# Kernel tuning notes

Measured on AMD Instinct MI355X. Metric: run time of the kernel, lower is better.

The kernel has to match this reference:

```python
import jax, jax.numpy as jnp
import numpy as np

N_NODES = 100_000
N_EDGES = 1_600_000
F_IN = 128
NHID = 128
G = 64            # num graphs in the batch
N_CLASSES = 2
EMB = NHID * 6    # embedding_data dim so concat dim == NHID*8


def _lin_init(k, fi, fo):
    s = 1.0 / np.sqrt(fi)
    k1, k2 = jax.random.split(k)
    w = jax.random.uniform(k1, (fi, fo), jnp.float32, -s, s)
    b = jax.random.uniform(k2, (fo,), jnp.float32, -s, s)
    return w, b


def setup_inputs() -> dict:
    key = jax.random.key(0)
    ks = jax.random.split(key, 12)
    x = jax.random.normal(ks[0], (N_NODES, F_IN), jnp.float32)
    edge_index = jax.random.randint(ks[1], (2, N_EDGES), 0, N_NODES, dtype=jnp.int32)
    per = N_NODES // G
    batch = jnp.minimum(jnp.arange(N_NODES, dtype=jnp.int32) // per, G - 1)  # sorted, even split
    embedding_data = jax.random.normal(ks[2], (G, EMB), jnp.float32)
    conv_w, conv_b = _lin_init(ks[3], F_IN, NHID)
    lin0_w, lin0_b = _lin_init(ks[4], F_IN, NHID)
    lin1_w, lin1_b = _lin_init(ks[5], NHID * 8, NHID * 4)
    lin2_w, lin2_b = _lin_init(ks[6], NHID * 4, NHID * 2)
    lin3_w, lin3_b = _lin_init(ks[7], NHID * 2, NHID)
    lin4_w, lin4_b = _lin_init(ks[8], NHID, N_CLASSES)
    return {
        "x": x, "embedding_data": embedding_data,
        "conv_w": conv_w, "conv_b": conv_b,
        "lin0_w": lin0_w, "lin0_b": lin0_b,
        "lin1_w": lin1_w, "lin1_b": lin1_b,
        "lin2_w": lin2_w, "lin2_b": lin2_b,
        "lin3_w": lin3_w, "lin3_b": lin3_b,
        "lin4_w": lin4_w, "lin4_b": lin4_b,
        "edge_index": edge_index, "batch": batch,
    }


def _gcn_conv(x, edge_index, w, b):
    """PyG GCNConv: add self-loops, symmetric deg^-1/2 normalization, linear, scatter-add."""
    n = x.shape[0]
    loop = jnp.arange(n, dtype=edge_index.dtype)
    src = jnp.concatenate([edge_index[0], loop])
    dst = jnp.concatenate([edge_index[1], loop])
    deg = jax.ops.segment_sum(jnp.ones_like(dst, dtype=x.dtype), dst, num_segments=n)
    dinv = jnp.where(deg > 0, jax.lax.rsqrt(deg), 0.0)
    norm = dinv[src] * dinv[dst]                     # [E+N]
    h = x @ w                                        # [N, NHID]
    msg = h[src] * norm[:, None]                     # gather  [E+N, NHID]
    out = jax.ops.segment_sum(msg, dst, num_segments=n)  # scatter-add
    return out + b


def reference(x, embedding_data, conv_w, conv_b, lin0_w, lin0_b,
              lin1_w, lin1_b, lin2_w, lin2_b, lin3_w, lin3_b,
              lin4_w, lin4_b, edge_index, batch):
    h = jax.nn.relu(_gcn_conv(x, edge_index, conv_w, conv_b))   # [N, NHID]
    pooled = jax.ops.segment_max(h, batch, num_segments=G)      # global max pool [G, NHID]
    # first node of each graph (batch is sorted)
    first_idx = jnp.searchsorted(batch, jnp.arange(G, dtype=batch.dtype))
    news = jax.nn.relu(x[first_idx] @ lin0_w + lin0_b)          # [G, NHID]
    z = jnp.concatenate([pooled, news, embedding_data], axis=1) # [G, NHID*8]
    z = jnp.tanh(z @ lin1_w + lin1_b)   # dropout = identity (eval mode)
    z = jnp.tanh(z @ lin2_w + lin2_b)
    z = jnp.tanh(z @ lin3_w + lin3_b)
    return jax.nn.log_softmax(z @ lin4_w + lin4_b, axis=-1)     # [G, N_CLASSES]
```

## Files before the change

### kernel.cpp

```cpp
#include <hip/hip_runtime.h>
#include <hip/hip_bf16.h>

#define N_NODES 100000
#define N_EDGES 1600000
#define F 128
#define G 64
#define EMB 768
#define PER 1562
#define CAP 96
#define NBUCK 256
#define BNODES 391
#define TILE 8192
#define NBIN 196
#define SLOT 80
#define GEMM_GRID 512
#define EWS_ENT 104

typedef __hip_bfloat16 bf16;
typedef __attribute__((ext_vector_type(8))) short short8;
typedef __attribute__((ext_vector_type(4))) float f32x4;
typedef unsigned int u32;

__device__ __forceinline__ float b2f(bf16 v) { return __bfloat162float(v); }
__device__ __forceinline__ short f2bs(float v) {
    bf16 b = __float2bfloat16(v);
    return *reinterpret_cast<short*>(&b);
}
__device__ __forceinline__ float bl16(u32 v) { return __uint_as_float(v << 16); }
__device__ __forceinline__ float bh16(u32 v) { return __uint_as_float(v & 0xffff0000u); }

__global__ void k_init(float* __restrict__ pooled) {
    int i = blockIdx.x * 256 + threadIdx.x;
    if (i < G * F) pooled[i] = 0.0f;
}

__global__ __launch_bounds__(256) void k_fat(const int* __restrict__ ei,
                                             int* __restrict__ cntarr,
                                             u32* __restrict__ stage,
                                             const float* __restrict__ x,
                                             const float* __restrict__ w,
                                             bf16* __restrict__ h) {
    int t = threadIdx.x;
    if (blockIdx.x < NBIN) {
        __shared__ int offs[NBUCK];
        offs[t] = 0;
        __syncthreads();
        int blk = blockIdx.x;
        int e0 = blk * TILE;
        int e1 = min(e0 + TILE, N_EDGES);
        for (int e = e0 + t; e < e1; e += 256) {
            int src = ei[e];
            int dst = ei[N_EDGES + e];
            int b = dst / BNODES;
            int dl = dst - b * BNODES;
            int pos = atomicAdd(&offs[b], 1);
            if (pos < SLOT)
                stage[((size_t)b * NBIN + blk) * SLOT + pos] = (u32)src | ((u32)dl << 17);
        }
        __syncthreads();
        cntarr[blk * NBUCK + t] = min(offs[t], SLOT);
    } else {
        __shared__ short wfrag[16384];
        for (int i = t; i < 16384; i += 256) {
            int j    = i & 7;
            int lane = (i >> 3) & 63;
            int kb   = (i >> 9) & 3;
            int ct   = i >> 11;
            int k    = kb * 32 + (lane >> 4) * 8 + j;
            int n    = ct * 16 + (lane & 15);
            wfrag[i] = f2bs(w[k * 128 + n]);
        }
        __syncthreads();

        int wv = t >> 6, lane = t & 63;
        int m = lane & 15, q = lane >> 4;
        int nchunks = (N_NODES + 63) / 64;
        for (int chunk = blockIdx.x - NBIN; chunk < nchunks; chunk += GEMM_GRID) {
            int row = chunk * 64 + wv * 16 + m;
            int rr = (row < N_NODES) ? row : 0;
            short8 a[4];
#pragma unroll
            for (int kb = 0; kb < 4; ++kb) {
                const float* src = x + (size_t)rr * F + kb * 32 + q * 8;
                float4 v0 = *(const float4*)src;
                float4 v1 = *(const float4*)(src + 4);
                short8 av;
                av[0] = f2bs(v0.x); av[1] = f2bs(v0.y); av[2] = f2bs(v0.z); av[3] = f2bs(v0.w);
                av[4] = f2bs(v1.x); av[5] = f2bs(v1.y); av[6] = f2bs(v1.z); av[7] = f2bs(v1.w);
                a[kb] = av;
            }
            f32x4 acc[8];
#pragma unroll
            for (int ct = 0; ct < 8; ++ct) {
                f32x4 c = {0.f, 0.f, 0.f, 0.f};
#pragma unroll
                for (int kb = 0; kb < 4; ++kb) {
                    short8 bfr = *(const short8*)&wfrag[((ct * 4 + kb) * 64 + lane) * 8];
                    c = __builtin_amdgcn_mfma_f32_16x16x32_bf16(a[kb], bfr, c, 0, 0, 0);
                }
                acc[ct] = c;
            }
            int rbase = chunk * 64 + wv * 16 + q * 4;
#pragma unroll
            for (int ct = 0; ct < 8; ++ct)
#pragma unroll
                for (int r = 0; r < 4; ++r) {
                    int ro = rbase + r;
                    if (ro < N_NODES) h[(size_t)ro * F + ct * 16 + m] = __float2bfloat16(acc[ct][r]);
                }
        }
    }
}

__global__ __launch_bounds__(1024) void k_scat(const u32* __restrict__ stage,
                                               const int* __restrict__ cntarr,
                                               int* __restrict__ cursor,
                                               float* __restrict__ dinv,
                                               int* __restrict__ slots) {
    __shared__ int lcur[BNODES];
    int b = blockIdx.x;
    int t = threadIdx.x;
    int wv = t >> 6, lane = t & 63;
    int nbase = b * BNODES;
    int bn = min(BNODES, N_NODES - nbase);
    if (bn <= 0) return;
    for (int l = t; l < bn; l += 1024) lcur[l] = 0;
    __syncthreads();
    for (int seg = wv; seg < NBIN; seg += 16) {
        int cnt = cntarr[seg * NBUCK + b];
        const u32* sp = stage + ((size_t)b * NBIN + seg) * SLOT;
        for (int i = lane; i < cnt; i += 64) {
            u32 p = sp[i];
            int src = (int)(p & 0x1FFFFu);
            int dl  = (int)(p >> 17);
            int pos = atomicAdd(&lcur[dl], 1);
            if (pos < CAP) slots[(size_t)(nbase + dl) * CAP + pos] = src;
        }
    }
    __syncthreads();
    for (int l = t; l < bn; l += 1024) {
        int c = lcur[l];
        cursor[nbase + l] = c;
        dinv[nbase + l] = rsqrtf((float)(c + 1));
    }
}

__global__ __launch_bounds__(256) void k_agg(const bf16* __restrict__ h,
                                             const float* __restrict__ dinv,
                                             const int* __restrict__ slots,
                                             const int* __restrict__ cnt,
                                             const float* __restrict__ cb,
                                             float* __restrict__ pooled) {
    __shared__ __align__(16) char smem[16 * EWS_ENT * 8];
    int2 (*ews)[EWS_ENT] = (int2(*)[EWS_ENT])smem;
    float (*red)[132] = (float(*)[132])smem;

    int t = threadIdx.x;
    int wv = t >> 6, lane = t & 63;
    int q  = lane >> 4;
    int fl = lane & 15;
    int nb = blockIdx.x * 16 + wv * 4;
    int node = nb + q;
    int row  = wv * 4 + q;

    int c0 = min(cnt[nb + 0], CAP), c1 = min(cnt[nb + 1], CAP);
    int c2 = min(cnt[nb + 2], CAP), c3 = min(cnt[nb + 3], CAP);
    int cq   = (q == 0) ? c0 : (q == 1) ? c1 : (q == 2) ? c2 : c3;
    int cmax = max(max(c0, c1), max(c2, c3));

    const int* slp = slots + (size_t)node * CAP;
#pragma unroll
    for (int k = 0; k < 7; ++k) {
        int j = k * 16 + fl;
        if (j < EWS_ENT) {
            int2 ew = {0, 0};
            if (j < cq) { int s = slp[j]; ew.x = s; ew.y = __float_as_int(dinv[s]); }
            ews[row][j] = ew;
        }
    }
    __syncthreads();

    float acc[8] = {0.f, 0.f, 0.f, 0.f, 0.f, 0.f, 0.f, 0.f};
    const uint4* ewv = (const uint4*)ews[row];
    const u32* hb = (const u32*)h;
    int fl4 = fl * 4;
    if (cmax > 0) {
        uint4 ea = ewv[0];
        uint4 eb = ewv[1];
        uint4 v0 = *(const uint4*)(hb + (size_t)ea.x * 64 + fl4);
        uint4 v1 = *(const uint4*)(hb + (size_t)ea.z * 64 + fl4);
        uint4 v2 = *(const uint4*)(hb + (size_t)eb.x * 64 + fl4);
        uint4 v3 = *(const uint4*)(hb + (size_t)eb.z * 64 + fl4);
        for (int s0 = 0; s0 < cmax; s0 += 4) {
            uint4 na = ewv[(s0 >> 1) + 2];
            uint4 nb4 = ewv[(s0 >> 1) + 3];
            uint4 n0 = *(const uint4*)(hb + (size_t)na.x * 64 + fl4);
            uint4 n1 = *(const uint4*)(hb + (size_t)na.z * 64 + fl4);
            uint4 n2 = *(const uint4*)(hb + (size_t)nb4.x * 64 + fl4);
            uint4 n3 = *(const uint4*)(hb + (size_t)nb4.z * 64 + fl4);
            float w0 = __uint_as_float(ea.y), w1 = __uint_as_float(ea.w);
            float w2 = __uint_as_float(eb.y), w3 = __uint_as_float(eb.w);
            acc[0] = fmaf(bl16(v0.x), w0, acc[0]);
            acc[1] = fmaf(bh16(v0.x), w0, acc[1]);
            acc[2] = fmaf(bl16(v0.y), w0, acc[2]);
            acc[3] = fmaf(bh16(v0.y), w0, acc[3]);
            acc[4] = fmaf(bl16(v0.z), w0, acc[4]);
            acc[5] = fmaf(bh16(v0.z), w0, acc[5]);
            acc[6] = fmaf(bl16(v0.w), w0, acc[6]);
            acc[7] = fmaf(bh16(v0.w), w0, acc[7]);
            acc[0] = fmaf(bl16(v1.x), w1, acc[0]);
            acc[1] = fmaf(bh16(v1.x), w1, acc[1]);
            acc[2] = fmaf(bl16(v1.y), w1, acc[2]);
            acc[3] = fmaf(bh16(v1.y), w1, acc[3]);
            acc[4] = fmaf(bl16(v1.z), w1, acc[4]);
            acc[5] = fmaf(bh16(v1.z), w1, acc[5]);
            acc[6] = fmaf(bl16(v1.w), w1, acc[6]);
            acc[7] = fmaf(bh16(v1.w), w1, acc[7]);
            acc[0] = fmaf(bl16(v2.x), w2, acc[0]);
            acc[1] = fmaf(bh16(v2.x), w2, acc[1]);
            acc[2] = fmaf(bl16(v2.y), w2, acc[2]);
            acc[3] = fmaf(bh16(v2.y), w2, acc[3]);
            acc[4] = fmaf(bl16(v2.z), w2, acc[4]);
            acc[5] = fmaf(bh16(v2.z), w2, acc[5]);
            acc[6] = fmaf(bl16(v2.w), w2, acc[6]);
            acc[7] = fmaf(bh16(v2.w), w2, acc[7]);
            acc[0] = fmaf(bl16(v3.x), w3, acc[0]);
            acc[1] = fmaf(bh16(v3.x), w3, acc[1]);
            acc[2] = fmaf(bl16(v3.y), w3, acc[2]);
            acc[3] = fmaf(bh16(v3.y), w3, acc[3]);
            acc[4] = fmaf(bl16(v3.z), w3, acc[4]);
            acc[5] = fmaf(bh16(v3.z), w3, acc[5]);
            acc[6] = fmaf(bl16(v3.w), w3, acc[6]);
            acc[7] = fmaf(bh16(v3.w), w3, acc[7]);
            ea = na; eb = nb4;
            v0 = n0; v1 = n1; v2 = n2; v3 = n3;
        }
    }

    float dn = dinv[node];
    float dn2 = dn * dn;
    uint4 hs = *(const uint4*)(hb + (size_t)node * 64 + fl4);
    float4 cbv0 = *(const float4*)&cb[8 * fl];
    float4 cbv1 = *(const float4*)&cb[8 * fl + 4];
    float s0v = fmaxf(fmaf(acc[0], dn, fmaf(bl16(hs.x), dn2, cbv0.x)), 0.f);
    float s1v = fmaxf(fmaf(acc[1], dn, fmaf(bh16(hs.x), dn2, cbv0.y)), 0.f);
    float s2v = fmaxf(fmaf(acc[2], dn, fmaf(bl16(hs.y), dn2, cbv0.z)), 0.f);
    float s3v = fmaxf(fmaf(acc[3], dn, fmaf(bh16(hs.y), dn2, cbv0.w)), 0.f);
    float s4v = fmaxf(fmaf(acc[4], dn, fmaf(bl16(hs.z), dn2, cbv1.x)), 0.f);
    float s5v = fmaxf(fmaf(acc[5], dn, fmaf(bh16(hs.z), dn2, cbv1.y)), 0.f);
    float s6v = fmaxf(fmaf(acc[6], dn, fmaf(bl16(hs.w), dn2, cbv1.z)), 0.f);
    float s7v = fmaxf(fmaf(acc[7], dn, fmaf(bh16(hs.w), dn2, cbv1.w)), 0.f);

    __syncthreads();
    *(float4*)&red[row][8 * fl]     = make_float4(s0v, s1v, s2v, s3v);
    *(float4*)&red[row][8 * fl + 4] = make_float4(s4v, s5v, s6v, s7v);
    __syncthreads();

    int n0 = blockIdx.x * 16;
    int g0 = min(n0 / PER, G - 1);
    int gL = min((n0 + 15) / PER, G - 1);
    if (g0 == gL) {
        if (wv == 0) {
            float m0 = red[0][2 * lane], m1 = red[0][2 * lane + 1];
#pragma unroll
            for (int r = 1; r < 16; ++r) {
                m0 = fmaxf(m0, red[r][2 * lane]);
                m1 = fmaxf(m1, red[r][2 * lane + 1]);
            }
            atomicMax((int*)&pooled[g0 * F + 2 * lane],     __float_as_int(m0));
            atomicMax((int*)&pooled[g0 * F + 2 * lane + 1], __float_as_int(m1));
        }
    } else {
#pragma unroll
        for (int r = 0; r < 4; ++r) {
            int rr = wv * 4 + r;
            int g = min((n0 + rr) / PER, G - 1);
            atomicMax((int*)&pooled[g * F + 2 * lane],     __float_as_int(red[rr][2 * lane]));
            atomicMax((int*)&pooled[g * F + 2 * lane + 1], __float_as_int(red[rr][2 * lane + 1]));
        }
    }
}

__global__ __launch_bounds__(256) void k_l1(const float* __restrict__ x,
                                            const float* __restrict__ pooled,
                                            const float* __restrict__ emb,
                                            const float* __restrict__ l0w,
                                            const float* __restrict__ l0b,
                                            const float* __restrict__ w1,
                                            const float* __restrict__ b1,
                                            float* __restrict__ z1) {
    int jc = blockIdx.x & 7;
    int g0 = (blockIdx.x >> 3) * 8;
    int t = threadIdx.x;
    __shared__ float zs[8][1024];
    __shared__ float xs[8][128];
    __shared__ float psum[4][8][64];
    for (int i = t; i < 8 * 128; i += 256) {
        int g = i >> 7, c = i & 127;
        zs[g][c] = pooled[(g0 + g) * 128 + c];
        xs[g][c] = x[(size_t)((g0 + g) * PER) * F + c];
    }
    for (int i = t; i < 8 * 768; i += 256) {
        int g = i / 768, c = i - g * 768;
        zs[g][256 + c] = emb[(g0 + g) * EMB + c];
    }
    __syncthreads();
    if (t < 128) {
        float nacc[8];
#pragma unroll
        for (int g = 0; g < 8; ++g) nacc[g] = l0b[t];
        for (int k = 0; k < 128; ++k) {
            float lw = l0w[k * 128 + t];
#pragma unroll
            for (int g = 0; g < 8; ++g) nacc[g] = fmaf(xs[g][k], lw, nacc[g]);
        }
#pragma unroll
        for (int g = 0; g < 8; ++g) zs[g][128 + t] = fmaxf(nacc[g], 0.f);
    }
    __syncthreads();
    int j = t & 63, kq = t >> 6;
    float acc[8] = {0.f, 0.f, 0.f, 0.f, 0.f, 0.f, 0.f, 0.f};
    const float* wp = w1 + (size_t)(kq * 256) * 512 + jc * 64 + j;
    for (int k = 0; k < 256; ++k) {
        float wv = wp[(size_t)k * 512];
        int kk = kq * 256 + k;
#pragma unroll
        for (int g = 0; g < 8; ++g) acc[g] = fmaf(zs[g][kk], wv, acc[g]);
    }
#pragma unroll
    for (int g = 0; g < 8; ++g) psum[kq][g][j] = acc[g];
    __syncthreads();
    for (int i = t; i < 512; i += 256) {
        int g = i >> 6, jj = i & 63;
        float s = b1[jc * 64 + jj] + psum[0][g][jj] + psum[1][g][jj]
                + psum[2][g][jj] + psum[3][g][jj];
        z1[(g0 + g) * 512 + jc * 64 + jj] = tanhf(s);
    }
}

__global__ __launch_bounds__(256) void k_l2(const float* __restrict__ z1,
                                            const float* __restrict__ w2,
                                            const float* __restrict__ b2,
                                            float* __restrict__ z2) {
    int jc = blockIdx.x & 3;
    int g0 = (blockIdx.x >> 2) * 8;
    int t = threadIdx.x;
    __shared__ float zs[8][512];
    __shared__ float psum[4][8][64];
    for (int i = t; i < 8 * 512; i += 256) {
        int g = i >> 9, c = i & 511;
        zs[g][c] = z1[(g0 + g) * 512 + c];
    }
    __syncthreads();
    int j = t & 63, kq = t >> 6;
    float acc[8] = {0.f, 0.f, 0.f, 0.f, 0.f, 0.f, 0.f, 0.f};
    const float* wp = w2 + (size_t)(kq * 128) * 256 + jc * 64 + j;
    for (int k = 0; k < 128; ++k) {
        float wv = wp[(size_t)k * 256];
        int kk = kq * 128 + k;
#pragma unroll
        for (int g = 0; g < 8; ++g) acc[g] = fmaf(zs[g][kk], wv, acc[g]);
    }
#pragma unroll
    for (int g = 0; g < 8; ++g) psum[kq][g][j] = acc[g];
    __syncthreads();
    for (int i = t; i < 512; i += 256) {
        int g = i >> 6, jj = i & 63;
        float s = b2[jc * 64 + jj] + psum[0][g][jj] + psum[1][g][jj]
                + psum[2][g][jj] + psum[3][g][jj];
        z2[(g0 + g) * 256 + jc * 64 + jj] = tanhf(s);
    }
}

__global__ __launch_bounds__(256) void k_l3out(const float* __restrict__ z2,
                                               const float* __restrict__ w3,
                                               const float* __restrict__ b3,
                                               const float* __restrict__ w4,
                                               const float* __restrict__ b4,
                                               float* __restrict__ out) {
    int g0 = blockIdx.x * 8;
    int t = threadIdx.x;
    __shared__ float zs[8][256];
    __shared__ float psum[2][8][128];
    __shared__ float z3s[8][128];
    __shared__ float logits[16];
    for (int i = t; i < 8 * 256; i += 256) {
        int g = i >> 8, c = i & 255;
        zs[g][c] = z2[(g0 + g) * 256 + c];
    }
    __syncthreads();
    int j = t & 127, kh = t >> 7;
    float acc[8] = {0.f, 0.f, 0.f, 0.f, 0.f, 0.f, 0.f, 0.f};
    const float* wp = w3 + (size_t)(kh * 128) * 128 + j;
    for (int k = 0; k < 128; ++k) {
        float wv = wp[(size_t)k * 128];
        int kk = kh * 128 + k;
#pragma unroll
        for (int g = 0; g < 8; ++g) acc[g] = fmaf(zs[g][kk], wv, acc[g]);
    }
#pragma unroll
    for (int g = 0; g < 8; ++g) psum[kh][g][j] = acc[g];
    __syncthreads();
    for (int i = t; i < 8 * 128; i += 256) {
        int g = i >> 7, jj = i & 127;
        z3s[g][jj] = tanhf(b3[jj] + psum[0][g][jj] + psum[1][g][jj]);
    }
    __syncthreads();
    if (t < 16) {
        int g = t >> 1, c = t & 1;
        float l = b4[c];
        for (int k = 0; k < 128; ++k) l += z3s[g][k] * w4[k * 2 + c];
        logits[t] = l;
    }
    __syncthreads();
    if (t < 8) {
        float l0 = logits[2 * t], l1 = logits[2 * t + 1];
        float m = fmaxf(l0, l1);
        float lse = m + logf(expf(l0 - m) + expf(l1 - m));
        out[(g0 + t) * 2 + 0] = l0 - lse;
        out[(g0 + t) * 2 + 1] = l1 - lse;
    }
}

extern "C" void kernel_launch(void* const* d_in, const int* in_sizes, int n_in,
                              void* d_out, int out_size, void* d_ws, size_t ws_size,
                              hipStream_t stream) {
    const float* x      = (const float*)d_in[0];
    const float* emb    = (const float*)d_in[1];
    const float* conv_w = (const float*)d_in[2];
    const float* conv_b = (const float*)d_in[3];
    const float* lin0_w = (const float*)d_in[4];
    const float* lin0_b = (const float*)d_in[5];
    const float* lin1_w = (const float*)d_in[6];
    const float* lin1_b = (const float*)d_in[7];
    const float* lin2_w = (const float*)d_in[8];
    const float* lin2_b = (const float*)d_in[9];
    const float* lin3_w = (const float*)d_in[10];
    const float* lin3_b = (const float*)d_in[11];
    const float* lin4_w = (const float*)d_in[12];
    const float* lin4_b = (const float*)d_in[13];
    const int*   ei     = (const int*)d_in[14];
    float* out = (float*)d_out;

    char* ws = (char*)d_ws;
    int*   cursor = (int*)ws;                         ws += (size_t)N_NODES * 4;
    float* dinv   = (float*)ws;                       ws += (size_t)N_NODES * 4;
    int*   slots  = (int*)ws;                         ws += (size_t)N_NODES * CAP * 4;
    bf16*  h      = (bf16*)ws;                        ws += (size_t)N_NODES * F * 2;
    float* pooled = (float*)ws;                       ws += (size_t)G * F * 4;
    int*   cntarr = (int*)ws;                         ws += (size_t)NBIN * NBUCK * 4;
    u32*   stage  = (u32*)ws;                         ws += (size_t)NBUCK * NBIN * SLOT * 4;
    float* z1     = (float*)ws;                       ws += (size_t)G * 512 * 4;
    float* z2     = (float*)ws;                       ws += (size_t)G * 256 * 4;

    k_init<<<(G * F + 255) / 256, 256, 0, stream>>>(pooled);
    k_fat<<<NBIN + GEMM_GRID, 256, 0, stream>>>(ei, cntarr, stage, x, conv_w, h);
    k_scat<<<NBUCK, 1024, 0, stream>>>(stage, cntarr, cursor, dinv, slots);
    k_agg<<<N_NODES / 16, 256, 0, stream>>>(h, dinv, slots, cursor, conv_b, pooled);
    k_l1<<<64, 256, 0, stream>>>(x, pooled, emb, lin0_w, lin0_b, lin1_w, lin1_b, z1);
    k_l2<<<32, 256, 0, stream>>>(z1, lin2_w, lin2_b, z2);
    k_l3out<<<8, 256, 0, stream>>>(z2, lin3_w, lin3_b, lin4_w, lin4_b, out);
}
```

Before: 306.3 us.

## Stage edge binning and slot lists in LDS for coalesced writes; fuse small kernels

Edge binning in k_fat becomes a two-pass LDS counting sort: it counts per bucket, runs a prefix scan, scatters into LDS, then copies each bucket to the stage buffer with contiguous writes. k_scat gets an LDS variant that builds per-node source lists (capacity 72) in about 114KB of dynamic shared memory and writes them out contiguously. If the larger shared memory cannot be enabled, it falls back to the old kernel. The pooled zeroing moves into the scatter kernel, and the lin2/lin3/out MLP kernels are fused into one launch. This trades extra LDS passes and less parallelism in the tiny MLP for fewer scattered global writes and fewer launches, but nodes with more than 72 in-edges would be truncated on the LDS path.

```diff
diff --git a/kernel.cpp b/kernel.cpp
--- a/kernel.cpp
+++ b/kernel.cpp
@@ -8,6 +8,7 @@
 #define EMB 768
 #define PER 1562
 #define CAP 96
+#define LCAP 72
 #define NBUCK 256
 #define BNODES 391
 #define TILE 8192
@@ -21,18 +22,12 @@
 typedef __attribute__((ext_vector_type(4))) float f32x4;
 typedef unsigned int u32;
 
-__device__ __forceinline__ float b2f(bf16 v) { return __bfloat162float(v); }
 __device__ __forceinline__ short f2bs(float v) {
     bf16 b = __float2bfloat16(v);
     return *reinterpret_cast<short*>(&b);
 }
 __device__ __forceinline__ float bl16(u32 v) { return __uint_as_float(v << 16); }
 __device__ __forceinline__ float bh16(u32 v) { return __uint_as_float(v & 0xffff0000u); }
-
-__global__ void k_init(float* __restrict__ pooled) {
-    int i = blockIdx.x * 256 + threadIdx.x;
-    if (i < G * F) pooled[i] = 0.0f;
-}
 
 __global__ __launch_bounds__(256) void k_fat(const int* __restrict__ ei,
                                              int* __restrict__ cntarr,
@@ -40,27 +35,63 @@
                                              const float* __restrict__ x,
                                              const float* __restrict__ w,
                                              bf16* __restrict__ h) {
+    __shared__ __align__(16) char smem[36864];
     int t = threadIdx.x;
     if (blockIdx.x < NBIN) {
-        __shared__ int offs[NBUCK];
-        offs[t] = 0;
-        __syncthreads();
+        u32* lbuf = (u32*)smem;
+        int* cnt  = (int*)(smem + 32768);
+        int* cur  = (int*)(smem + 33792);
+        int* offs = (int*)(smem + 34816);
         int blk = blockIdx.x;
         int e0 = blk * TILE;
         int e1 = min(e0 + TILE, N_EDGES);
+        cnt[t] = 0;
+        __syncthreads();
+        for (int e = e0 + t; e < e1; e += 256) {
+            int dst = ei[N_EDGES + e];
+            atomicAdd(&cnt[dst / BNODES], 1);
+        }
+        __syncthreads();
+        if (t < 64) {
+            int base = t * 4;
+            int c0 = cnt[base], c1 = cnt[base + 1], c2 = cnt[base + 2], c3 = cnt[base + 3];
+            int s = c0 + c1 + c2 + c3;
+            int xv = s;
+#pragma unroll
+            for (int d = 1; d < 64; d <<= 1) {
+                int y = __shfl_up(xv, d);
+                if (t >= d) xv += y;
+            }
+            int excl = xv - s;
+            offs[base]     = excl;
+            offs[base + 1] = excl + c0;
+            offs[base + 2] = excl + c0 + c1;
+            offs[base + 3] = excl + c0 + c1 + c2;
+            cur[base]     = offs[base];
+            cur[base + 1] = offs[base + 1];
+            cur[base + 2] = offs[base + 2];
+            cur[base + 3] = offs[base + 3];
+        }
+        __syncthreads();
         for (int e = e0 + t; e < e1; e += 256) {
             int src = ei[e];
             int dst = ei[N_EDGES + e];
             int b = dst / BNODES;
             int dl = dst - b * BNODES;
-            int pos = atomicAdd(&offs[b], 1);
-            if (pos < SLOT)
-                stage[((size_t)b * NBIN + blk) * SLOT + pos] = (u32)src | ((u32)dl << 17);
-        }
-        __syncthreads();
-        cntarr[blk * NBUCK + t] = min(offs[t], SLOT);
+            int pos = atomicAdd(&cur[b], 1);
+            lbuf[pos] = (u32)src | ((u32)dl << 17);
+        }
+        __syncthreads();
+        int wv = t >> 6, lane = t & 63;
+        for (int b = wv; b < NBUCK; b += 4) {
+            int s0 = offs[b];
+            int c = min(cnt[b], SLOT);
+            u32* dp = stage + ((size_t)b * NBIN + blk) * SLOT;
+            for (int j = lane; j < c; j += 64) dp[j] = lbuf[s0 + j];
+        }
+        cntarr[blk * NBUCK + t] = min(cnt[t], SLOT);
     } else {
-        __shared__ short wfrag[16384];
+        short* wfrag = (short*)smem;
         for (int i = t; i < 16384; i += 256) {
             int j    = i & 7;
             int lane = (i >> 3) & 63;
@@ -112,11 +143,54 @@
     }
 }
 
-__global__ __launch_bounds__(1024) void k_scat(const u32* __restrict__ stage,
-                                               const int* __restrict__ cntarr,
-                                               int* __restrict__ cursor,
-                                               float* __restrict__ dinv,
-                                               int* __restrict__ slots) {
+__global__ __launch_bounds__(1024) void k_scat_lds(const u32* __restrict__ stage,
+                                                   const int* __restrict__ cntarr,
+                                                   int* __restrict__ cursor,
+                                                   float* __restrict__ dinv,
+                                                   int* __restrict__ slots,
+                                                   float* __restrict__ pooled) {
+    extern __shared__ int dls[];
+    int* lsl  = dls;
+    int* lcur = dls + BNODES * LCAP;
+    int b = blockIdx.x;
+    int t = threadIdx.x;
+    int wv = t >> 6, lane = t & 63;
+    int nbase = b * BNODES;
+    int bn = min(BNODES, N_NODES - nbase);
+    if (bn <= 0) return;
+    if (b == 0) for (int i = t; i < G * F; i += 1024) pooled[i] = 0.f;
+    for (int l = t; l < bn; l += 1024) lcur[l] = 0;
+    __syncthreads();
+    for (int seg = wv; seg < NBIN; seg += 16) {
+        int cv = cntarr[seg * NBUCK + b];
+        const u32* sp = stage + ((size_t)b * NBIN + seg) * SLOT;
+        for (int i = lane; i < cv; i += 64) {
+            u32 p = sp[i];
+            int src = (int)(p & 0x1FFFFu);
+            int dl  = (int)(p >> 17);
+            int pos = atomicAdd(&lcur[dl], 1);
+            if (pos < LCAP) lsl[dl * LCAP + pos] = src;
+        }
+    }
+    __syncthreads();
+    for (int l = wv; l < bn; l += 16) {
+        int c = lcur[l];
+        int cc = min(c, LCAP);
+        int* dp = slots + (size_t)(nbase + l) * CAP;
+        for (int j = lane; j < cc; j += 64) dp[j] = lsl[l * LCAP + j];
+        if (lane == 0) {
+            cursor[nbase + l] = c;
+            dinv[nbase + l] = rsqrtf((float)(c + 1));
+        }
+    }
+}
+
+__global__ __launch_bounds__(1024) void k_scat_fb(const u32* __restrict__ stage,
+                                                  const int* __restrict__ cntarr,
+                                                  int* __restrict__ cursor,
+                                                  float* __restrict__ dinv,
+                                                  int* __restrict__ slots,
+                                                  float* __restrict__ pooled) {
     __shared__ int lcur[BNODES];
     int b = blockIdx.x;
     int t = threadIdx.x;
@@ -124,6 +198,7 @@
     int nbase = b * BNODES;
     int bn = min(BNODES, N_NODES - nbase);
     if (bn <= 0) return;
+    if (b == 0) for (int i = t; i < G * F; i += 1024) pooled[i] = 0.f;
     for (int l = t; l < bn; l += 1024) lcur[l] = 0;
     __syncthreads();
     for (int seg = wv; seg < NBIN; seg += 16) {
@@ -338,72 +413,63 @@
     }
 }
 
-__global__ __launch_bounds__(256) void k_l2(const float* __restrict__ z1,
-                                            const float* __restrict__ w2,
-                                            const float* __restrict__ b2,
-                                            float* __restrict__ z2) {
-    int jc = blockIdx.x & 3;
-    int g0 = (blockIdx.x >> 2) * 8;
+__global__ __launch_bounds__(256) void k_l23(const float* __restrict__ z1,
+                                             const float* __restrict__ w2,
+                                             const float* __restrict__ b2,
+                                             const float* __restrict__ w3,
+                                             const float* __restrict__ b3,
+                                             const float* __restrict__ w4,
+                                             const float* __restrict__ b4,
+                                             float* __restrict__ out) {
+    int g0 = blockIdx.x * 8;
     int t = threadIdx.x;
     __shared__ float zs[8][512];
-    __shared__ float psum[4][8][64];
+    __shared__ float z2s[8][256];
+    __shared__ float ps[4][8][64];
+    __shared__ float ps3[2][8][128];
+    __shared__ float z3s[8][128];
+    __shared__ float logits[16];
     for (int i = t; i < 8 * 512; i += 256) {
         int g = i >> 9, c = i & 511;
         zs[g][c] = z1[(g0 + g) * 512 + c];
     }
     __syncthreads();
     int j = t & 63, kq = t >> 6;
-    float acc[8] = {0.f, 0.f, 0.f, 0.f, 0.f, 0.f, 0.f, 0.f};
-    const float* wp = w2 + (size_t)(kq * 128) * 256 + jc * 64 + j;
+    for (int jc = 0; jc < 4; ++jc) {
+        float acc[8] = {0.f, 0.f, 0.f, 0.f, 0.f, 0.f, 0.f, 0.f};
+        const float* wp = w2 + (size_t)(kq * 128) * 256 + jc * 64 + j;
+        for (int k = 0; k < 128; ++k) {
+            float wv2 = wp[(size_t)k * 256];
+            int kk = kq * 128 + k;
+#pragma unroll
+            for (int g = 0; g < 8; ++g) acc[g] = fmaf(zs[g][kk], wv2, acc[g]);
+        }
+#pragma unroll
+        for (int g = 0; g < 8; ++g) ps[kq][g][j] = acc[g];
+        __syncthreads();
+        for (int i = t; i < 512; i += 256) {
+            int g = i >> 6, jj = i & 63;
+            float s = b2[jc * 64 + jj] + ps[0][g][jj] + ps[1][g][jj]
+                    + ps[2][g][jj] + ps[3][g][jj];
+            z2s[g][jc * 64 + jj] = tanhf(s);
+        }
+        __syncthreads();
+    }
+    int j2 = t & 127, kh = t >> 7;
+    float acc3[8] = {0.f, 0.f, 0.f, 0.f, 0.f, 0.f, 0.f, 0.f};
+    const float* wp3 = w3 + (size_t)(kh * 128) * 128 + j2;
     for (int k = 0; k < 128; ++k) {
-        float wv = wp[(size_t)k * 256];
-        int kk = kq * 128 + k;
-#pragma unroll
-        for (int g = 0; g < 8; ++g) acc[g] = fmaf(zs[g][kk], wv, acc[g]);
-    }
-#pragma unroll
-    for (int g = 0; g < 8; ++g) psum[kq][g][j] = acc[g];
-    __syncthreads();
-    for (int i = t; i < 512; i += 256) {
-        int g = i >> 6, jj = i & 63;
-        float s = b2[jc * 64 + jj] + psum[0][g][jj] + psum[1][g][jj]
-                + psum[2][g][jj] + psum[3][g][jj];
-        z2[(g0 + g) * 256 + jc * 64 + jj] = tanhf(s);
-    }
-}
-
-__global__ __launch_bounds__(256) void k_l3out(const float* __restrict__ z2,
-                                               const float* __restrict__ w3,
-                                               const float* __restrict__ b3,
-                                               const float* __restrict__ w4,
-                                               const float* __restrict__ b4,
-                                               float* __restrict__ out) {
-    int g0 = blockIdx.x * 8;
-    int t = threadIdx.x;
-    __shared__ float zs[8][256];
-    __shared__ float psum[2][8][128];
-    __shared__ float z3s[8][128];
-    __shared__ float logits[16];
-    for (int i = t; i < 8 * 256; i += 256) {
-        int g = i >> 8, c = i & 255;
-        zs[g][c] = z2[(g0 + g) * 256 + c];
-    }
-    __syncthreads();
-    int j = t & 127, kh = t >> 7;
-    float acc[8] = {0.f, 0.f, 0.f, 0.f, 0.f, 0.f, 0.f, 0.f};
-    const float* wp = w3 + (size_t)(kh * 128) * 128 + j;
-    for (int k = 0; k < 128; ++k) {
-        float wv = wp[(size_t)k * 128];
+        float wv3 = wp3[(size_t)k * 128];
         int kk = kh * 128 + k;
 #pragma unroll
-        for (int g = 0; g < 8; ++g) acc[g] = fmaf(zs[g][kk], wv, acc[g]);
-    }
-#pragma unroll
-    for (int g = 0; g < 8; ++g) psum[kh][g][j] = acc[g];
+        for (int g = 0; g < 8; ++g) acc3[g] = fmaf(z2s[g][kk], wv3, acc3[g]);
+    }
+#pragma unroll
+    for (int g = 0; g < 8; ++g) ps3[kh][g][j2] = acc3[g];
     __syncthreads();
     for (int i = t; i < 8 * 128; i += 256) {
         int g = i >> 7, jj = i & 127;
-        z3s[g][jj] = tanhf(b3[jj] + psum[0][g][jj] + psum[1][g][jj]);
+        z3s[g][jj] = tanhf(b3[jj] + ps3[0][g][jj] + ps3[1][g][jj]);
     }
     __syncthreads();
     if (t < 16) {
@@ -452,12 +518,22 @@
     u32*   stage  = (u32*)ws;                         ws += (size_t)NBUCK * NBIN * SLOT * 4;
     float* z1     = (float*)ws;                       ws += (size_t)G * 512 * 4;
     float* z2     = (float*)ws;                       ws += (size_t)G * 256 * 4;
-
-    k_init<<<(G * F + 255) / 256, 256, 0, stream>>>(pooled);
+    (void)z2;
+
+    static int scat_mode = 0;
+    const int DYN = (BNODES * LCAP + BNODES) * 4;
+    if (scat_mode == 0) {
+        scat_mode = (hipFuncSetAttribute((const void*)k_scat_lds,
+                        hipFuncAttributeMaxDynamicSharedMemorySize, DYN) == hipSuccess)
+                    ? 1 : 2;
+    }
+
     k_fat<<<NBIN + GEMM_GRID, 256, 0, stream>>>(ei, cntarr, stage, x, conv_w, h);
-    k_scat<<<NBUCK, 1024, 0, stream>>>(stage, cntarr, cursor, dinv, slots);
+    if (scat_mode == 1)
+        k_scat_lds<<<NBUCK, 1024, DYN, stream>>>(stage, cntarr, cursor, dinv, slots, pooled);
+    else
+        k_scat_fb<<<NBUCK, 1024, 0, stream>>>(stage, cntarr, cursor, dinv, slots, pooled);
     k_agg<<<N_NODES / 16, 256, 0, stream>>>(h, dinv, slots, cursor, conv_b, pooled);
     k_l1<<<64, 256, 0, stream>>>(x, pooled, emb, lin0_w, lin0_b, lin1_w, lin1_b, z1);
-    k_l2<<<32, 256, 0, stream>>>(z1, lin2_w, lin2_b, z2);
-    k_l3out<<<8, 256, 0, stream>>>(z2, lin3_w, lin3_b, lin4_w, lin4_b, out);
-}
+    k_l23<<<8, 256, 0, stream>>>(z1, lin2_w, lin2_b, lin3_w, lin3_b, lin4_w, lin4_b, out);
+}
```

After: 326.8 us. 1.07x slower.
